# Kernel tuning notes

Measured on AMD Instinct MI355X. Metric: run time of the kernel, lower is better.

## Reference

```python
import jax, jax.numpy as jnp
from jax import lax
import numpy as np

B, S, T, I, H, O = 128, 144, 50, 10, 64, 1


def setup_inputs() -> dict:
    key = jax.random.key(0)
    ks = jax.random.split(key, 11)
    sI = 1.0 / np.sqrt(H)
    x = jax.random.normal(ks[0], (B, S, T, I), dtype=jnp.float32)
    # PyTorch nn.GRU weights per direction: W_ih [3H,I], W_hh [3H,H], b_ih [3H], b_hh [3H]
    Wih_f = jax.random.normal(ks[1], (T, 3 * H, I), dtype=jnp.float32) * sI
    Whh_f = jax.random.normal(ks[2], (T, 3 * H, H), dtype=jnp.float32) * sI
    bih_f = jax.random.normal(ks[3], (T, 3 * H), dtype=jnp.float32) * sI
    bhh_f = jax.random.normal(ks[4], (T, 3 * H), dtype=jnp.float32) * sI
    Wih_b = jax.random.normal(ks[5], (T, 3 * H, I), dtype=jnp.float32) * sI
    Whh_b = jax.random.normal(ks[6], (T, 3 * H, H), dtype=jnp.float32) * sI
    bih_b = jax.random.normal(ks[7], (T, 3 * H), dtype=jnp.float32) * sI
    bhh_b = jax.random.normal(ks[8], (T, 3 * H), dtype=jnp.float32) * sI
    Wfc = jax.random.normal(ks[9], (T, O, 2 * H), dtype=jnp.float32) * sI
    bfc = jax.random.normal(ks[10], (T, O), dtype=jnp.float32) * sI
    return {"x": x, "Wih_f": Wih_f, "Whh_f": Whh_f, "bih_f": bih_f, "bhh_f": bhh_f,
            "Wih_b": Wih_b, "Whh_b": Whh_b, "bih_b": bih_b, "bhh_b": bhh_b,
            "Wfc": Wfc, "bfc": bfc}


def _gru_cell(x_t, h, Wih, Whh, bih, bhh):
    # PyTorch GRU cell math
    gi = x_t @ Wih.T + bih          # [B, 3H]
    gh = h @ Whh.T + bhh            # [B, 3H]
    i_r, i_z, i_n = jnp.split(gi, 3, axis=-1)
    h_r, h_z, h_n = jnp.split(gh, 3, axis=-1)
    r = jax.nn.sigmoid(i_r + h_r)
    z = jax.nn.sigmoid(i_z + h_z)
    n = jnp.tanh(i_n + r * h_n)
    return (1.0 - z) * n + z * h


def _per_turbine(xt, wih_f, whh_f, bih_f, bhh_f, wih_b, whh_b, bih_b, bhh_b, wfc, bfc):
    # xt: [B, S, I]
    x_sbi = jnp.transpose(xt, (1, 0, 2))  # [S, B, I]
    h0 = jnp.zeros((xt.shape[0], H), xt.dtype)

    def step(h, x_t):
        h = _gru_cell(x_t, h, wih_f, whh_f, bih_f, bhh_f)
        return h, None

    hf, _ = lax.scan(step, h0, x_sbi)  # forward final hidden = fwd output at t=S-1
    # backward-direction output at last timestep = first step of the reverse scan
    hb = _gru_cell(xt[:, -1, :], h0, wih_b, whh_b, bih_b, bhh_b)
    h = jnp.concatenate([hf, hb], axis=-1)  # [B, 2H]; dropout is identity at inference
    return h @ wfc.T + bfc  # [B, O]


def reference(x, Wih_f, Whh_f, bih_f, bhh_f, Wih_b, Whh_b, bih_b, bhh_b, Wfc, bfc):
    x_tbsi = jnp.transpose(x, (2, 0, 1, 3))  # [T, B, S, I]
    out = jax.vmap(_per_turbine)(x_tbsi, Wih_f, Whh_f, bih_f, bhh_f,
                                 Wih_b, Whh_b, bih_b, bhh_b, Wfc, bfc)  # [T, B, O]
    return jnp.transpose(out, (1, 2, 0))  # [B, O, T]
```

## Files before the change

### kernel.cpp

```cpp
#include <hip/hip_runtime.h>


typedef _Float16 f16;
typedef _Float16 f16x8 __attribute__((ext_vector_type(8)));
typedef float    f32x4 __attribute__((ext_vector_type(4)));

constexpr int B_N = 128, S_N = 144, T_N = 50, I_N = 10, H_N = 64, G3 = 192;
constexpr int BT = 16, NB = B_N / BT;
constexpr int HST = 88;
constexpr float L2E = 1.44269504089f;

#define MFMA16(a, b, c) __builtin_amdgcn_mfma_f32_16x16x32_f16((a), (b), (c), 0, 0, 0)

__device__ __forceinline__ float fsig(float v) {
    return __builtin_amdgcn_rcpf(1.0f + __builtin_amdgcn_exp2f(-L2E * v));
}
__device__ __forceinline__ float ftanh(float v) {
    return 1.0f - 2.0f * __builtin_amdgcn_rcpf(1.0f + __builtin_amdgcn_exp2f(2.0f * L2E * v));
}

__global__ __launch_bounds__(256)
void pack_x(const float* __restrict__ x, f16* __restrict__ xP) {
    const int idx = blockIdx.x * 256 + threadIdx.x;
    if (idx >= B_N * S_N * T_N) return;
    const float* s = x + (size_t)idx * I_N;
    f16x8 lo, hi;
    #pragma unroll
    for (int e = 0; e < 8; ++e) lo[e] = (f16)s[e];
    hi[0] = (f16)s[8]; hi[1] = (f16)s[9]; hi[2] = (f16)1.0f;
    #pragma unroll
    for (int e = 3; e < 8; ++e) hi[e] = (f16)0.0f;
    f16* d = xP + (size_t)idx * 16;
    *(f16x8*)d = lo; *(f16x8*)(d + 8) = hi;
}

#define LOADX_P(ss, xf)                                                           \
    if ((ss) < S_N && lg < 2)                                                     \
        xf = *(const f16x8*)(xProw + (size_t)(ss) * (T_N * 16) + lg * 8);

#define LOADX_R(ss, q0, q1, q2, q3, q4)                                           \
    if ((ss) < S_N) {                                                             \
        const float* _p = x + (((size_t)(b0 + lc) * S_N + (ss)) * T_N + t) * I_N; \
        if (lg == 0) {                                                            \
            q0 = *(const float2*)(_p);     q1 = *(const float2*)(_p + 2);         \
            q2 = *(const float2*)(_p + 4); q3 = *(const float2*)(_p + 6);         \
        } else if (lg == 1) {                                                     \
            q4 = *(const float2*)(_p + 8);                                        \
        }                                                                         \
    }

#define STEP(ss, xf, q0, q1, q2, q3, q4)                                          \
    {                                                                             \
        const int cur = (ss) & 1, nxt = cur ^ 1;                                  \
        const f16* hrow = &hL[cur][lc][0];                                        \
        const f16x8 hA0 = *(const f16x8*)(hrow + lg * 8);                         \
        const f16x8 hA1 = *(const f16x8*)(hrow + 32 + lg * 8);                    \
        f16x8 xA;                                                                 \
        if constexpr (PX) {                                                       \
            xA = xf;                                                              \
            LOADX_P((ss) + 2, xf)                                                 \
        } else {                                                                  \
            _Pragma("unroll")                                                     \
            for (int e = 0; e < 8; ++e) xA[e] = (f16)0.0f;                        \
            if (lg == 0) {                                                        \
                xA[0] = (f16)q0.x; xA[1] = (f16)q0.y; xA[2] = (f16)q1.x; xA[3] = (f16)q1.y; \
                xA[4] = (f16)q2.x; xA[5] = (f16)q2.y; xA[6] = (f16)q3.x; xA[7] = (f16)q3.y; \
            } else if (lg == 1) {                                                 \
                xA[0] = (f16)q4.x; xA[1] = (f16)q4.y; xA[2] = (f16)1.0f;          \
            }                                                                     \
            LOADX_R((ss) + 2, q0, q1, q2, q3, q4)                                 \
        }                                                                         \
        f32x4 aR  = {0.f, 0.f, 0.f, 0.f};                                         \
        f32x4 aZ  = {0.f, 0.f, 0.f, 0.f};                                         \
        f32x4 aNH = {0.f, 0.f, 0.f, 0.f};                                         \
        f32x4 aNX = {0.f, 0.f, 0.f, 0.f};                                         \
        aR  = MFMA16(xA,  BxR,  aR);                                              \
        aZ  = MFMA16(xA,  BxZ,  aZ);                                              \
        aNX = MFMA16(xA,  BxN,  aNX);                                             \
        aR  = MFMA16(hA0, BhR0, aR);                                              \
        aR  = MFMA16(hA1, BhR1, aR);                                              \
        aZ  = MFMA16(hA0, BhZ0, aZ);                                              \
        aZ  = MFMA16(hA1, BhZ1, aZ);                                              \
        aNH = MFMA16(hA0, BhN0, aNH);                                             \
        aNH = MFMA16(hA1, BhN1, aNH);                                             \
        const int r0 = lg * 4;                                                    \
        _Pragma("unroll")                                                         \
        for (int j = 0; j < 4; ++j) {                                             \
            const float rr = __builtin_amdgcn_rcpf(1.0f + __builtin_amdgcn_exp2f(aR[j])); \
            const float zz = __builtin_amdgcn_rcpf(1.0f + __builtin_amdgcn_exp2f(aZ[j])); \
            const float qq = __builtin_amdgcn_rcpf(1.0f + __builtin_amdgcn_exp2f(fmaf(rr, aNH[j] + bnhs, aNX[j]))); \
            const float nn = fmaf(-2.0f, qq, 1.0f);                               \
            ho[j] = fmaf(zz, ho[j] - nn, nn);                                     \
            hL[nxt][r0 + j][uc + lc] = (f16)ho[j];                                \
        }                                                                         \
        asm volatile("s_waitcnt lgkmcnt(0)" ::: "memory");                        \
        __builtin_amdgcn_s_barrier();                                             \
        asm volatile("" ::: "memory");                                            \
    }

template<bool PX>
__global__ __launch_bounds__(256, 2)
void gru_mfma(const float* __restrict__ x, const f16* __restrict__ xP,
              const float* __restrict__ Wih_f, const float* __restrict__ Whh_f,
              const float* __restrict__ bih_f, const float* __restrict__ bhh_f,
              const float* __restrict__ Wih_b, const float* __restrict__ bih_b,
              const float* __restrict__ bhh_b,
              const float* __restrict__ Wfc,   const float* __restrict__ bfc,
              float* __restrict__ out)
{
    __shared__ f16   hL[2][BT][HST];
    __shared__ float hfL[BT][H_N + 1];
    __shared__ float hbL[BT][H_N + 1];

    const int tid = threadIdx.x;
    const int w   = tid >> 6, l = tid & 63;
    const int uc  = w * 16;
    const int lc  = l & 15;
    const int lg  = l >> 4;
    const int t   = blockIdx.x / NB;
    const int b0  = (blockIdx.x % NB) * BT;

    {
        f16* hp = &hL[0][0][0];
        for (int i = tid; i < BT * HST; i += 256) hp[i] = (f16)0.0f;
    }

    const float* Whh = Whh_f + (size_t)t * G3 * H_N;
    const float* Wih = Wih_f + (size_t)t * G3 * I_N;
    const f16*  xProw = PX ? (xP + ((size_t)(b0 + lc) * S_N * T_N + t) * 16) : nullptr;

    const float sRZ = -L2E, sN = 2.0f * L2E;
    auto loadBh = [&](int g, int kk, float sc) -> f16x8 {
        const float4* p = (const float4*)(Whh + (size_t)g * H_N + kk * 32 + lg * 8);
        const float4 a = p[0], b = p[1];
        f16x8 v;
        v[0] = (f16)(sc * a.x); v[1] = (f16)(sc * a.y); v[2] = (f16)(sc * a.z); v[3] = (f16)(sc * a.w);
        v[4] = (f16)(sc * b.x); v[5] = (f16)(sc * b.y); v[6] = (f16)(sc * b.z); v[7] = (f16)(sc * b.w);
        return v;
    };
    auto loadBx = [&](int g, bool rz, float sc) -> f16x8 {
        f16x8 v;
        #pragma unroll
        for (int j = 0; j < 8; ++j) {
            const int k = lg * 8 + j;
            float val = 0.0f;
            if (k < I_N)       val = Wih[(size_t)g * I_N + k];
            else if (k == 10)  val = bih_f[t * G3 + g] + (rz ? bhh_f[t * G3 + g] : 0.0f);
            v[j] = (f16)(sc * val);
        }
        return v;
    };

    const f16x8 BhR0 = loadBh(uc + lc, 0, sRZ),        BhR1 = loadBh(uc + lc, 1, sRZ);
    const f16x8 BhZ0 = loadBh(64 + uc + lc, 0, sRZ),   BhZ1 = loadBh(64 + uc + lc, 1, sRZ);
    const f16x8 BhN0 = loadBh(128 + uc + lc, 0, sN),   BhN1 = loadBh(128 + uc + lc, 1, sN);
    const f16x8 BxR  = loadBx(uc + lc, true, sRZ);
    const f16x8 BxZ  = loadBx(64 + uc + lc, true, sRZ);
    const f16x8 BxN  = loadBx(128 + uc + lc, false, sN);
    const float bnhs = sN * bhh_f[t * G3 + 128 + uc + lc];

    f16x8 xpA, xpB;
    #pragma unroll
    for (int e = 0; e < 8; ++e) { xpA[e] = (f16)0.0f; xpB[e] = (f16)0.0f; }
    float2 ra0 = {0.f,0.f}, ra1 = {0.f,0.f}, ra2 = {0.f,0.f}, ra3 = {0.f,0.f}, ra4 = {0.f,0.f};
    float2 rb0 = {0.f,0.f}, rb1 = {0.f,0.f}, rb2 = {0.f,0.f}, rb3 = {0.f,0.f}, rb4 = {0.f,0.f};
    if constexpr (PX) {
        LOADX_P(0, xpA)
        LOADX_P(1, xpB)
    } else {
        LOADX_R(0, ra0, ra1, ra2, ra3, ra4)
        LOADX_R(1, rb0, rb1, rb2, rb3, rb4)
    }

    float ho[4] = {0.f, 0.f, 0.f, 0.f};

    __syncthreads();

    for (int s = 0; s < S_N; s += 2) {
        STEP(s,     xpA, ra0, ra1, ra2, ra3, ra4)
        STEP(s + 1, xpB, rb0, rb1, rb2, rb3, rb4)
    }

    {
        const int r0 = lg * 4;
        hfL[r0 + 0][uc + lc] = ho[0];
        hfL[r0 + 1][uc + lc] = ho[1];
        hfL[r0 + 2][uc + lc] = ho[2];
        hfL[r0 + 3][uc + lc] = ho[3];
    }

    {
        const int row2 = tid >> 4;
        const int j0   = (tid & 15) * 4;
        const float* wib = Wih_b + (size_t)t * G3 * I_N;
        const float* bib = bih_b + t * G3;
        const float* bhb = bhh_b + t * G3;
        float xr[I_N];
        #pragma unroll
        for (int k = 0; k < I_N; ++k)
            xr[k] = x[(((size_t)(b0 + row2) * S_N + (S_N - 1)) * T_N + t) * I_N + k];
        #pragma unroll
        for (int m = 0; m < 4; ++m) {
            const int j = j0 + m;
            float ir = bib[j], iz = bib[64 + j], inn = bib[128 + j];
            #pragma unroll
            for (int k = 0; k < I_N; ++k) {
                const float xv = xr[k];
                ir  += wib[(size_t)j * I_N + k]          * xv;
                iz  += wib[(size_t)(64 + j) * I_N + k]   * xv;
                inn += wib[(size_t)(128 + j) * I_N + k]  * xv;
            }
            const float r  = fsig(ir + bhb[j]);
            const float z  = fsig(iz + bhb[64 + j]);
            const float nn = ftanh(inn + r * bhb[128 + j]);
            hbL[row2][j] = (1.0f - z) * nn;
        }
    }
    __syncthreads();

    if (tid < BT) {
        const float* wfc = Wfc + (size_t)t * 2 * H_N;
        float acc = bfc[t];
        #pragma unroll 4
        for (int j = 0; j < H_N; ++j) acc += hfL[tid][j] * wfc[j];
        #pragma unroll 4
        for (int j = 0; j < H_N; ++j) acc += hbL[tid][j] * wfc[64 + j];
        out[(size_t)(b0 + tid) * T_N + t] = acc;
    }
}

extern "C" void kernel_launch(void* const* d_in, const int* in_sizes, int n_in,
                              void* d_out, int out_size, void* d_ws, size_t ws_size,
                              hipStream_t stream) {
    const float* x     = (const float*)d_in[0];
    const float* Wih_f = (const float*)d_in[1];
    const float* Whh_f = (const float*)d_in[2];
    const float* bih_f = (const float*)d_in[3];
    const float* bhh_f = (const float*)d_in[4];
    const float* Wih_b = (const float*)d_in[5];
    const float* bih_b = (const float*)d_in[7];
    const float* bhh_b = (const float*)d_in[8];
    const float* Wfc   = (const float*)d_in[9];
    const float* bfc   = (const float*)d_in[10];
    float* out = (float*)d_out;

    const size_t xp_bytes = (size_t)B_N * S_N * T_N * 16 * sizeof(f16);
    dim3 grid(T_N * NB), block(256);

    if (ws_size >= xp_bytes) {
        f16* xP = (f16*)d_ws;
        const int n = B_N * S_N * T_N;
        hipLaunchKernelGGL(pack_x, dim3((n + 255) / 256), dim3(256), 0, stream, x, xP);
        hipLaunchKernelGGL((gru_mfma<true>), grid, block, 0, stream,
                           x, xP, Wih_f, Whh_f, bih_f, bhh_f, Wih_b, bih_b, bhh_b, Wfc, bfc, out);
    } else {
        hipLaunchKernelGGL((gru_mfma<false>), grid, block, 0, stream,
                           x, nullptr, Wih_f, Whh_f, bih_f, bhh_f, Wih_b, bih_b, bhh_b, Wfc, bfc, out);
    }
}
```

Before: 102.4 us.

## Process two batch tiles per block to interleave independent GRU recurrences

The packed-input path now gives each block 32 batch rows, run as two independent 16-row recurrences whose MFMAs and gate math are interleaved inside one barrier per step. The grid shrinks from 400 to 200 blocks, so per-step barrier and latency costs are shared across two chains and can overlap. The gate math also merges the z and n reciprocals into one rcp of a product. The trade-off is fewer blocks on a 256-CU device (under one per CU), more registers per thread, and launch bounds relaxed to one block per CU.

```diff
diff --git a/kernel.cpp b/kernel.cpp
--- a/kernel.cpp
+++ b/kernel.cpp
@@ -6,7 +6,7 @@
 typedef float    f32x4 __attribute__((ext_vector_type(4)));
 
 constexpr int B_N = 128, S_N = 144, T_N = 50, I_N = 10, H_N = 64, G3 = 192;
-constexpr int BT = 16, NB = B_N / BT;
+constexpr int BT = 16;
 constexpr int HST = 88;
 constexpr float L2E = 1.44269504089f;
 
@@ -34,9 +34,189 @@
     *(f16x8*)d = lo; *(f16x8*)(d + 8) = hi;
 }
 
-#define LOADX_P(ss, xf)                                                           \
-    if ((ss) < S_N && lg < 2)                                                     \
-        xf = *(const f16x8*)(xProw + (size_t)(ss) * (T_N * 16) + lg * 8);
+#define GATES(j, aR, aZ, aNH, aNX, ho, sIdx)                                      \
+    {                                                                             \
+        const float eA = __builtin_amdgcn_exp2f(aR[j]);                           \
+        const float eB = __builtin_amdgcn_exp2f(aZ[j]);                           \
+        const float rr = __builtin_amdgcn_rcpf(1.0f + eA);                        \
+        const float eC = __builtin_amdgcn_exp2f(fmaf(rr, aNH[j] + bnhs, aNX[j])); \
+        const float t1 = 1.0f + eB, t2 = 1.0f + eC;                               \
+        const float ip = __builtin_amdgcn_rcpf(t1 * t2);                          \
+        const float zz = t2 * ip, qq = t1 * ip;                                   \
+        const float nn = fmaf(-2.0f, qq, 1.0f);                                   \
+        ho[j] = fmaf(zz, ho[j] - nn, nn);                                         \
+        hL[sIdx][nxt][r0 + (j)][uc + lc] = (f16)ho[j];                            \
+    }
+
+#define STEP2(ss, f0, f1)                                                         \
+    {                                                                             \
+        const int cur = (ss) & 1, nxt = cur ^ 1;                                  \
+        const f16* hr0 = &hL[0][cur][lc][0];                                      \
+        const f16* hr1 = &hL[1][cur][lc][0];                                      \
+        const f16x8 hA00 = *(const f16x8*)(hr0 + lg * 8);                         \
+        const f16x8 hA01 = *(const f16x8*)(hr0 + 32 + lg * 8);                    \
+        const f16x8 hA10 = *(const f16x8*)(hr1 + lg * 8);                         \
+        const f16x8 hA11 = *(const f16x8*)(hr1 + 32 + lg * 8);                    \
+        const f16x8 xA0 = f0, xA1 = f1;                                           \
+        if ((ss) + 2 < S_N && lg < 2) {                                           \
+            f0 = *(const f16x8*)(xProw0 + (size_t)((ss) + 2) * (T_N * 16) + lg * 8); \
+            f1 = *(const f16x8*)(xProw1 + (size_t)((ss) + 2) * (T_N * 16) + lg * 8); \
+        }                                                                         \
+        f32x4 aR0 = {0,0,0,0}, aZ0 = {0,0,0,0}, aNH0 = {0,0,0,0}, aNX0 = {0,0,0,0}; \
+        f32x4 aR1 = {0,0,0,0}, aZ1 = {0,0,0,0}, aNH1 = {0,0,0,0}, aNX1 = {0,0,0,0}; \
+        aR0  = MFMA16(xA0,  BxR,  aR0);   aR1  = MFMA16(xA1,  BxR,  aR1);         \
+        aZ0  = MFMA16(xA0,  BxZ,  aZ0);   aZ1  = MFMA16(xA1,  BxZ,  aZ1);         \
+        aNX0 = MFMA16(xA0,  BxN,  aNX0);  aNX1 = MFMA16(xA1,  BxN,  aNX1);        \
+        aR0  = MFMA16(hA00, BhR0, aR0);   aR1  = MFMA16(hA10, BhR0, aR1);         \
+        aR0  = MFMA16(hA01, BhR1, aR0);   aR1  = MFMA16(hA11, BhR1, aR1);         \
+        aZ0  = MFMA16(hA00, BhZ0, aZ0);   aZ1  = MFMA16(hA10, BhZ0, aZ1);         \
+        aZ0  = MFMA16(hA01, BhZ1, aZ0);   aZ1  = MFMA16(hA11, BhZ1, aZ1);         \
+        aNH0 = MFMA16(hA00, BhN0, aNH0);  aNH1 = MFMA16(hA10, BhN0, aNH1);        \
+        aNH0 = MFMA16(hA01, BhN1, aNH0);  aNH1 = MFMA16(hA11, BhN1, aNH1);        \
+        const int r0 = lg * 4;                                                    \
+        _Pragma("unroll")                                                         \
+        for (int j = 0; j < 4; ++j) {                                             \
+            GATES(j, aR0, aZ0, aNH0, aNX0, ho0, 0)                                \
+            GATES(j, aR1, aZ1, aNH1, aNX1, ho1, 1)                                \
+        }                                                                         \
+        asm volatile("s_waitcnt lgkmcnt(0)" ::: "memory");                        \
+        __builtin_amdgcn_s_barrier();                                             \
+        asm volatile("" ::: "memory");                                            \
+    }
+
+__global__ __launch_bounds__(256, 1)
+void gru_mfma2(const float* __restrict__ x, const f16* __restrict__ xP,
+               const float* __restrict__ Wih_f, const float* __restrict__ Whh_f,
+               const float* __restrict__ bih_f, const float* __restrict__ bhh_f,
+               const float* __restrict__ Wih_b, const float* __restrict__ bih_b,
+               const float* __restrict__ bhh_b,
+               const float* __restrict__ Wfc,   const float* __restrict__ bfc,
+               float* __restrict__ out)
+{
+    __shared__ f16   hL[2][2][BT][HST];
+    __shared__ float hfL[2 * BT][H_N + 1];
+    __shared__ float hbL[2 * BT][H_N + 1];
+
+    const int tid = threadIdx.x;
+    const int w   = tid >> 6, l = tid & 63;
+    const int uc  = w * 16;
+    const int lc  = l & 15;
+    const int lg  = l >> 4;
+    const int t   = blockIdx.x >> 2;
+    const int b0  = (blockIdx.x & 3) * 32;
+
+    {
+        f16* hp = &hL[0][0][0][0];
+        for (int i = tid; i < 2 * 2 * BT * HST; i += 256) hp[i] = (f16)0.0f;
+    }
+
+    const float* Whh = Whh_f + (size_t)t * G3 * H_N;
+    const float* Wih = Wih_f + (size_t)t * G3 * I_N;
+    const f16* xProw0 = xP + ((size_t)(b0 + lc) * S_N * T_N + t) * 16;
+    const f16* xProw1 = xP + ((size_t)(b0 + 16 + lc) * S_N * T_N + t) * 16;
+
+    const float sRZ = -L2E, sN = 2.0f * L2E;
+    auto loadBh = [&](int g, int kk, float sc) -> f16x8 {
+        const float4* p = (const float4*)(Whh + (size_t)g * H_N + kk * 32 + lg * 8);
+        const float4 a = p[0], b = p[1];
+        f16x8 v;
+        v[0] = (f16)(sc * a.x); v[1] = (f16)(sc * a.y); v[2] = (f16)(sc * a.z); v[3] = (f16)(sc * a.w);
+        v[4] = (f16)(sc * b.x); v[5] = (f16)(sc * b.y); v[6] = (f16)(sc * b.z); v[7] = (f16)(sc * b.w);
+        return v;
+    };
+    auto loadBx = [&](int g, bool rz, float sc) -> f16x8 {
+        f16x8 v;
+        #pragma unroll
+        for (int j = 0; j < 8; ++j) {
+            const int k = lg * 8 + j;
+            float val = 0.0f;
+            if (k < I_N)       val = Wih[(size_t)g * I_N + k];
+            else if (k == 10)  val = bih_f[t * G3 + g] + (rz ? bhh_f[t * G3 + g] : 0.0f);
+            v[j] = (f16)(sc * val);
+        }
+        return v;
+    };
+
+    const f16x8 BhR0 = loadBh(uc + lc, 0, sRZ),        BhR1 = loadBh(uc + lc, 1, sRZ);
+    const f16x8 BhZ0 = loadBh(64 + uc + lc, 0, sRZ),   BhZ1 = loadBh(64 + uc + lc, 1, sRZ);
+    const f16x8 BhN0 = loadBh(128 + uc + lc, 0, sN),   BhN1 = loadBh(128 + uc + lc, 1, sN);
+    const f16x8 BxR  = loadBx(uc + lc, true, sRZ);
+    const f16x8 BxZ  = loadBx(64 + uc + lc, true, sRZ);
+    const f16x8 BxN  = loadBx(128 + uc + lc, false, sN);
+    const float bnhs = sN * bhh_f[t * G3 + 128 + uc + lc];
+
+    f16x8 xs0a, xs0b, xs1a, xs1b;
+    #pragma unroll
+    for (int e = 0; e < 8; ++e) { xs0a[e] = (f16)0.0f; xs0b[e] = (f16)0.0f;
+                                  xs1a[e] = (f16)0.0f; xs1b[e] = (f16)0.0f; }
+    if (lg < 2) {
+        xs0a = *(const f16x8*)(xProw0 + lg * 8);
+        xs1a = *(const f16x8*)(xProw1 + lg * 8);
+        xs0b = *(const f16x8*)(xProw0 + (size_t)(T_N * 16) + lg * 8);
+        xs1b = *(const f16x8*)(xProw1 + (size_t)(T_N * 16) + lg * 8);
+    }
+
+    float ho0[4] = {0.f, 0.f, 0.f, 0.f};
+    float ho1[4] = {0.f, 0.f, 0.f, 0.f};
+
+    __syncthreads();
+
+    for (int s = 0; s < S_N; s += 2) {
+        STEP2(s,     xs0a, xs1a)
+        STEP2(s + 1, xs0b, xs1b)
+    }
+
+    {
+        const int r0 = lg * 4;
+        #pragma unroll
+        for (int j = 0; j < 4; ++j) {
+            hfL[r0 + j][uc + lc]      = ho0[j];
+            hfL[16 + r0 + j][uc + lc] = ho1[j];
+        }
+    }
+
+    {
+        const int row2 = tid >> 3;
+        const int j0   = (tid & 7) * 8;
+        const float* wib = Wih_b + (size_t)t * G3 * I_N;
+        const float* bib = bih_b + t * G3;
+        const float* bhb = bhh_b + t * G3;
+        float2 xr[5];
+        const float2* xp2 = (const float2*)(x + (((size_t)(b0 + row2) * S_N + (S_N - 1)) * T_N + t) * I_N);
+        #pragma unroll
+        for (int k = 0; k < 5; ++k) xr[k] = xp2[k];
+        #pragma unroll
+        for (int m = 0; m < 8; ++m) {
+            const int j = j0 + m;
+            float ir = bib[j], iz = bib[64 + j], inn = bib[128 + j];
+            const float2* wr = (const float2*)(wib + (size_t)j * I_N);
+            const float2* wz = (const float2*)(wib + (size_t)(64 + j) * I_N);
+            const float2* wn = (const float2*)(wib + (size_t)(128 + j) * I_N);
+            #pragma unroll
+            for (int k = 0; k < 5; ++k) {
+                ir  = fmaf(wr[k].x, xr[k].x, fmaf(wr[k].y, xr[k].y, ir));
+                iz  = fmaf(wz[k].x, xr[k].x, fmaf(wz[k].y, xr[k].y, iz));
+                inn = fmaf(wn[k].x, xr[k].x, fmaf(wn[k].y, xr[k].y, inn));
+            }
+            const float r  = fsig(ir + bhb[j]);
+            const float z  = fsig(iz + bhb[64 + j]);
+            const float nn = ftanh(inn + r * bhb[128 + j]);
+            hbL[row2][j] = (1.0f - z) * nn;
+        }
+    }
+    __syncthreads();
+
+    if (tid < 2 * BT) {
+        const float* wfc = Wfc + (size_t)t * 2 * H_N;
+        float acc = bfc[t];
+        #pragma unroll 4
+        for (int j = 0; j < H_N; ++j) acc += hfL[tid][j] * wfc[j];
+        #pragma unroll 4
+        for (int j = 0; j < H_N; ++j) acc += hbL[tid][j] * wfc[64 + j];
+        out[(size_t)(b0 + tid) * T_N + t] = acc;
+    }
+}
+
 
 #define LOADX_R(ss, q0, q1, q2, q3, q4)                                           \
     if ((ss) < S_N) {                                                             \
@@ -49,31 +229,23 @@
         }                                                                         \
     }
 
-#define STEP(ss, xf, q0, q1, q2, q3, q4)                                          \
+#define STEP1(ss, q0, q1, q2, q3, q4)                                             \
     {                                                                             \
         const int cur = (ss) & 1, nxt = cur ^ 1;                                  \
         const f16* hrow = &hL[cur][lc][0];                                        \
         const f16x8 hA0 = *(const f16x8*)(hrow + lg * 8);                         \
         const f16x8 hA1 = *(const f16x8*)(hrow + 32 + lg * 8);                    \
         f16x8 xA;                                                                 \
-        if constexpr (PX) {                                                       \
-            xA = xf;                                                              \
-            LOADX_P((ss) + 2, xf)                                                 \
-        } else {                                                                  \
-            _Pragma("unroll")                                                     \
-            for (int e = 0; e < 8; ++e) xA[e] = (f16)0.0f;                        \
-            if (lg == 0) {                                                        \
-                xA[0] = (f16)q0.x; xA[1] = (f16)q0.y; xA[2] = (f16)q1.x; xA[3] = (f16)q1.y; \
-                xA[4] = (f16)q2.x; xA[5] = (f16)q2.y; xA[6] = (f16)q3.x; xA[7] = (f16)q3.y; \
-            } else if (lg == 1) {                                                 \
-                xA[0] = (f16)q4.x; xA[1] = (f16)q4.y; xA[2] = (f16)1.0f;          \
-            }                                                                     \
-            LOADX_R((ss) + 2, q0, q1, q2, q3, q4)                                 \
+        _Pragma("unroll")                                                         \
+        for (int e = 0; e < 8; ++e) xA[e] = (f16)0.0f;                            \
+        if (lg == 0) {                                                            \
+            xA[0] = (f16)q0.x; xA[1] = (f16)q0.y; xA[2] = (f16)q1.x; xA[3] = (f16)q1.y; \
+            xA[4] = (f16)q2.x; xA[5] = (f16)q2.y; xA[6] = (f16)q3.x; xA[7] = (f16)q3.y; \
+        } else if (lg == 1) {                                                     \
+            xA[0] = (f16)q4.x; xA[1] = (f16)q4.y; xA[2] = (f16)1.0f;              \
         }                                                                         \
-        f32x4 aR  = {0.f, 0.f, 0.f, 0.f};                                         \
-        f32x4 aZ  = {0.f, 0.f, 0.f, 0.f};                                         \
-        f32x4 aNH = {0.f, 0.f, 0.f, 0.f};                                         \
-        f32x4 aNX = {0.f, 0.f, 0.f, 0.f};                                         \
+        LOADX_R((ss) + 2, q0, q1, q2, q3, q4)                                     \
+        f32x4 aR  = {0,0,0,0}, aZ = {0,0,0,0}, aNH = {0,0,0,0}, aNX = {0,0,0,0};  \
         aR  = MFMA16(xA,  BxR,  aR);                                              \
         aZ  = MFMA16(xA,  BxZ,  aZ);                                              \
         aNX = MFMA16(xA,  BxN,  aNX);                                             \
@@ -98,15 +270,14 @@
         asm volatile("" ::: "memory");                                            \
     }
 
-template<bool PX>
 __global__ __launch_bounds__(256, 2)
-void gru_mfma(const float* __restrict__ x, const f16* __restrict__ xP,
-              const float* __restrict__ Wih_f, const float* __restrict__ Whh_f,
-              const float* __restrict__ bih_f, const float* __restrict__ bhh_f,
-              const float* __restrict__ Wih_b, const float* __restrict__ bih_b,
-              const float* __restrict__ bhh_b,
-              const float* __restrict__ Wfc,   const float* __restrict__ bfc,
-              float* __restrict__ out)
+void gru_mfma1(const float* __restrict__ x,
+               const float* __restrict__ Wih_f, const float* __restrict__ Whh_f,
+               const float* __restrict__ bih_f, const float* __restrict__ bhh_f,
+               const float* __restrict__ Wih_b, const float* __restrict__ bih_b,
+               const float* __restrict__ bhh_b,
+               const float* __restrict__ Wfc,   const float* __restrict__ bfc,
+               float* __restrict__ out)
 {
     __shared__ f16   hL[2][BT][HST];
     __shared__ float hfL[BT][H_N + 1];
@@ -117,17 +288,16 @@
     const int uc  = w * 16;
     const int lc  = l & 15;
     const int lg  = l >> 4;
-    const int t   = blockIdx.x / NB;
-    const int b0  = (blockIdx.x % NB) * BT;
+    const int t   = blockIdx.x >> 3;
+    const int b0  = (blockIdx.x & 7) * BT;
 
     {
         f16* hp = &hL[0][0][0];
-        for (int i = tid; i < BT * HST; i += 256) hp[i] = (f16)0.0f;
+        for (int i = tid; i < 2 * BT * HST; i += 256) hp[i] = (f16)0.0f;
     }
 
     const float* Whh = Whh_f + (size_t)t * G3 * H_N;
     const float* Wih = Wih_f + (size_t)t * G3 * I_N;
-    const f16*  xProw = PX ? (xP + ((size_t)(b0 + lc) * S_N * T_N + t) * 16) : nullptr;
 
     const float sRZ = -L2E, sN = 2.0f * L2E;
     auto loadBh = [&](int g, int kk, float sc) -> f16x8 {
@@ -159,34 +329,24 @@
     const f16x8 BxN  = loadBx(128 + uc + lc, false, sN);
     const float bnhs = sN * bhh_f[t * G3 + 128 + uc + lc];
 
-    f16x8 xpA, xpB;
-    #pragma unroll
-    for (int e = 0; e < 8; ++e) { xpA[e] = (f16)0.0f; xpB[e] = (f16)0.0f; }
     float2 ra0 = {0.f,0.f}, ra1 = {0.f,0.f}, ra2 = {0.f,0.f}, ra3 = {0.f,0.f}, ra4 = {0.f,0.f};
     float2 rb0 = {0.f,0.f}, rb1 = {0.f,0.f}, rb2 = {0.f,0.f}, rb3 = {0.f,0.f}, rb4 = {0.f,0.f};
-    if constexpr (PX) {
-        LOADX_P(0, xpA)
-        LOADX_P(1, xpB)
-    } else {
-        LOADX_R(0, ra0, ra1, ra2, ra3, ra4)
-        LOADX_R(1, rb0, rb1, rb2, rb3, rb4)
-    }
+    LOADX_R(0, ra0, ra1, ra2, ra3, ra4)
+    LOADX_R(1, rb0, rb1, rb2, rb3, rb4)
 
     float ho[4] = {0.f, 0.f, 0.f, 0.f};
 
     __syncthreads();
 
     for (int s = 0; s < S_N; s += 2) {
-        STEP(s,     xpA, ra0, ra1, ra2, ra3, ra4)
-        STEP(s + 1, xpB, rb0, rb1, rb2, rb3, rb4)
+        STEP1(s,     ra0, ra1, ra2, ra3, ra4)
+        STEP1(s + 1, rb0, rb1, rb2, rb3, rb4)
     }
 
     {
         const int r0 = lg * 4;
-        hfL[r0 + 0][uc + lc] = ho[0];
-        hfL[r0 + 1][uc + lc] = ho[1];
-        hfL[r0 + 2][uc + lc] = ho[2];
-        hfL[r0 + 3][uc + lc] = ho[3];
+        #pragma unroll
+        for (int j = 0; j < 4; ++j) hfL[r0 + j][uc + lc] = ho[j];
     }
 
     {
@@ -245,16 +405,15 @@
     float* out = (float*)d_out;
 
     const size_t xp_bytes = (size_t)B_N * S_N * T_N * 16 * sizeof(f16);
-    dim3 grid(T_N * NB), block(256);
 
     if (ws_size >= xp_bytes) {
         f16* xP = (f16*)d_ws;
         const int n = B_N * S_N * T_N;
         hipLaunchKernelGGL(pack_x, dim3((n + 255) / 256), dim3(256), 0, stream, x, xP);
-        hipLaunchKernelGGL((gru_mfma<true>), grid, block, 0, stream,
+        hipLaunchKernelGGL(gru_mfma2, dim3(T_N * 4), dim3(256), 0, stream,
                            x, xP, Wih_f, Whh_f, bih_f, bhh_f, Wih_b, bih_b, bhh_b, Wfc, bfc, out);
     } else {
-        hipLaunchKernelGGL((gru_mfma<false>), grid, block, 0, stream,
-                           x, nullptr, Wih_f, Whh_f, bih_f, bhh_f, Wih_b, bih_b, bhh_b, Wfc, bfc, out);
-    }
-}
+        hipLaunchKernelGGL(gru_mfma1, dim3(T_N * 8), dim3(256), 0, stream,
+                           x, Wih_f, Whh_f, bih_f, bhh_f, Wih_b, bih_b, bhh_b, Wfc, bfc, out);
+    }
+}
```

New measurement: 136.3 us. 33.0% more time.
